# Kernel tuning notes

Measured on AMD Instinct MI355X. Metric: run time of the kernel, lower is better.

The kernel has to match this reference:

```python
import jax, jax.numpy as jnp
from jax import lax
import numpy as np

# GConv2d config (matches init_kwargs)
OUT_TRANSFORMS = 4  # rotations: 0, 90, 180, 270 degrees
STRIDE = 1
PADDING = 1


def setup_inputs() -> dict:
    key = jax.random.key(0)
    k1, k2, k3, k4 = jax.random.split(key, 4)
    B, IC_EFF, H, W = 16, 256, 64, 64   # IC_EFF = in_channels * in_transformations
    OC, K, F = 64, 4, 3                 # out_channels, num_dynamic_kernels, filter_size
    x = jax.random.normal(k1, (B, IC_EFF, H, W), dtype=jnp.float32)
    W_fc = jax.random.normal(k2, (K, IC_EFF), dtype=jnp.float32) * (1.0 / np.sqrt(IC_EFF))
    b_fc = jnp.zeros((K,), dtype=jnp.float32)
    kernel_bank = jax.random.normal(k3, (K, OC, IC_EFF, F, F), dtype=jnp.float32)
    return {"x": x, "W_fc": W_fc, "b_fc": b_fc, "kernel_bank": kernel_bank}


def reference(x, W_fc, b_fc, kernel_bank):
    B, C, H, W = x.shape
    # Dynamic routing: global average pool -> linear -> softmax over kernel bank
    pooled = x.mean(axis=(2, 3))                      # [B, C]
    coeffs = jax.nn.softmax(pooled @ W_fc.T + b_fc, axis=1)  # [B, K]
    # Sample-specific base kernels: mix of kernel bank
    base = jnp.einsum('bk,kocij->bocij', coeffs, kernel_bank)  # [B, oc, C, f, f]
    # P4 orientation expansion: rotate kernel spatially, stack along out-channels
    oriented = jnp.concatenate(
        [jnp.rot90(base, k, axes=(-2, -1)) for k in range(OUT_TRANSFORMS)], axis=1
    )  # [B, 4*oc, C, f, f]
    O, f = oriented.shape[1], oriented.shape[-1]
    # Batched per-sample conv via grouped convolution (one launch instead of B)
    xg = x.reshape(1, B * C, H, W)
    kg = oriented.reshape(B * O, C, f, f)
    out = lax.conv_general_dilated(
        xg, kg,
        window_strides=(STRIDE, STRIDE),
        padding=[(PADDING, PADDING), (PADDING, PADDING)],
        dimension_numbers=('NCHW', 'OIHW', 'NCHW'),
        feature_group_count=B,
    )  # [1, B*O, H', W']
    Ho, Wo = out.shape[-2], out.shape[-1]
    return out.reshape(B, O, Ho, Wo)
```

## Files before the change

kernel.cpp:

```cpp
#include <hip/hip_runtime.h>

#define B_  16
#define C_  256
#define OC_ 64
#define O_  256

typedef short    bf16x8 __attribute__((ext_vector_type(8)));
typedef float    f32x16 __attribute__((ext_vector_type(16)));
typedef unsigned u32x4  __attribute__((ext_vector_type(4)));
typedef unsigned u32x2  __attribute__((ext_vector_type(2)));

#define RT8   8
#define XR    10
#define XC    66
#define XTILE (XR*2*XC*8)
#define WTILE (9*2*64*8)
#define WORP_PER WTILE
#define WORP_BYTES ((size_t)B_*16*4*WORP_PER*2)

__device__ __forceinline__ unsigned cvtpk(float lo, float hi) {
    unsigned r;
    asm("v_cvt_pk_bf16_f32 %0, %1, %2" : "=v"(r) : "v"(lo), "v"(hi));
    return r;
}

__device__ __forceinline__ void gload16(const void* g, void* l) {
    __builtin_amdgcn_global_load_lds(
        (const __attribute__((address_space(1))) unsigned int*)g,
        (__attribute__((address_space(3))) unsigned int*)l, 16, 0, 0);
}

__global__ __launch_bounds__(256) void pool_kernel(const float* __restrict__ x,
                                                   float* __restrict__ pooled) {
    int bc = blockIdx.x;
    const float4* p = (const float4*)(x + (size_t)bc * 4096);
    float s = 0.f;
#pragma unroll
    for (int i = 0; i < 4; ++i) {
        float4 v = p[threadIdx.x + 256 * i];
        s += v.x + v.y + v.z + v.w;
    }
#pragma unroll
    for (int off = 32; off; off >>= 1) s += __shfl_down(s, off, 64);
    __shared__ float red[4];
    int lane = threadIdx.x & 63, wid = threadIdx.x >> 6;
    if (lane == 0) red[wid] = s;
    __syncthreads();
    if (threadIdx.x == 0)
        pooled[bc] = (red[0] + red[1] + red[2] + red[3]) * (1.0f / 4096.0f);
}

__global__ __launch_bounds__(256) void mix_kernel(const float* __restrict__ bank,
                                                  const float* __restrict__ pooled,
                                                  const float* __restrict__ W_fc,
                                                  const float* __restrict__ b_fc,
                                                  short* __restrict__ worp) {
    const int b  = blockIdx.x;
    const int cc = blockIdx.y;
    const int t  = threadIdx.x, lane = t & 63, wid = t >> 6;

    __shared__ float bankL[4 * 64 * 37];
    __shared__ float lg[4];

    {
        float s = 0.f;
#pragma unroll
        for (int q = 0; q < 4; ++q) {
            int c = lane * 4 + q;
            s += pooled[b * C_ + c] * W_fc[wid * C_ + c];
        }
#pragma unroll
        for (int off = 32; off; off >>= 1) s += __shfl_down(s, off, 64);
        if (lane == 0) lg[wid] = s + b_fc[wid];
    }
    __syncthreads();
    float l0 = lg[0], l1 = lg[1], l2 = lg[2], l3 = lg[3];
    float mx = fmaxf(fmaxf(l0, l1), fmaxf(l2, l3));
    float e0 = expf(l0 - mx), e1 = expf(l1 - mx), e2 = expf(l2 - mx), e3 = expf(l3 - mx);
    float inv = 1.f / (e0 + e1 + e2 + e3);
    const float cf0 = e0 * inv, cf1 = e1 * inv, cf2 = e2 * inv, cf3 = e3 * inv;

    const int oq  = t >> 6;
    const int o64 = t & 63;

    for (int sub = 0; sub < 4; ++sub) {
        __syncthreads();
        for (int i = t; i < 9216; i += 256) {
            int run = i / 36, e = i % 36;
            bankL[run * 37 + e] = bank[((size_t)run * C_ + cc * 16 + sub * 4) * 9 + e];
        }
        __syncthreads();

        const int lhs = sub >> 1;
        const float* bp = &bankL[o64 * 37];
#pragma unroll
        for (int ti = 0; ti < 3; ++ti)
#pragma unroll
            for (int tj = 0; tj < 3; ++tj) {
                int si, sj;
                if      (oq == 0) { si = ti;     sj = tj;     }
                else if (oq == 1) { si = tj;     sj = 2 - ti; }
                else if (oq == 2) { si = 2 - ti; sj = 2 - tj; }
                else              { si = 2 - tj; sj = ti;     }
                const int sij = si * 3 + sj;
                float v[4];
#pragma unroll
                for (int c4 = 0; c4 < 4; ++c4) {
                    const float* q = bp + c4 * 9 + sij;
                    v[c4] = cf0 * q[0] + cf1 * q[64 * 37] + cf2 * q[2 * 64 * 37]
                          + cf3 * q[3 * 64 * 37];
                }
                u32x2 d = { cvtpk(v[0], v[1]), cvtpk(v[2], v[3]) };
                size_t base = (((((size_t)(b * 16 + cc) * 4 + oq) * 9 + (ti * 3 + tj)) * 2
                                + lhs) * 64 + o64) * 8 + (sub & 1) * 4;
                *(u32x2*)&worp[base] = d;
            }
    }
}

__global__ __launch_bounds__(256, 2)
void conv_mfma(const float* __restrict__ x, const short* __restrict__ worp,
               float* __restrict__ out) {
    __shared__ short xls[XTILE];
    __shared__ short wls[2 * WTILE];

    const int g    = blockIdx.x;
    const int w    = (g & 7) * 64 + (g >> 3);
    const int oq   = w & 3;
    const int m    = w >> 2;
    const int rowt = m & 7;
    const int b    = m >> 3;
    const int y0   = rowt * RT8;

    const int t    = threadIdx.x;
    const int lane = t & 63;
    const int wid  = t >> 6;
    const int l31  = lane & 31;
    const int lh   = lane >> 5;

    const float* xb  = x + ((size_t)b << 20);
    const short* wbB = worp + ((size_t)(b * 16) * 4 + oq) * WORP_PER;

    int  goff[3], lb[3];
    bool act[3], inb[3];
#pragma unroll
    for (int si = 0; si < 3; ++si) {
        int s = t + si * 256;
        act[si] = (s < XR * XC);
        int r = s / XC, col = s % XC;
        int y = y0 + r - 1, gx = col - 1;
        inb[si]  = act[si] && (unsigned)y < 64 && (unsigned)gx < 64;
        goff[si] = y * 64 + gx;
        lb[si]   = ((r * 2) * XC + col) * 8;
    }
    float xf0[16], xf1[16], xf2[16];

#define LOADSLOT(xf, si, ccc)                                                   \
    { const float* p = xb + ((size_t)(ccc) << 16) + goff[si];                   \
      _Pragma("unroll")                                                         \
      for (int ci = 0; ci < 16; ++ci) xf[ci] = inb[si] ? p[(size_t)ci << 12] : 0.f; }

#define WRITESLOT(xf, si)                                                       \
    if (act[si]) {                                                              \
        u32x4 dA = { cvtpk(xf[0], xf[1]),  cvtpk(xf[2], xf[3]),                 \
                     cvtpk(xf[4], xf[5]),  cvtpk(xf[6], xf[7]) };               \
        u32x4 dB = { cvtpk(xf[8], xf[9]),  cvtpk(xf[10], xf[11]),               \
                     cvtpk(xf[12], xf[13]), cvtpk(xf[14], xf[15]) };            \
        *(u32x4*)&xls[lb[si]]          = dA;                                    \
        *(u32x4*)&xls[lb[si] + XC * 8] = dB;                                    \
    }

#define GLOADW(ccc, par)                                                        \
    { const char* wsrc = (const char*)(wbB + (size_t)(ccc) * (4 * WORP_PER));   \
      char* wdst = (char*)(wls + (par) * WTILE);                                \
      for (int u = wid; u < 18; u += 4)                                         \
          gload16(wsrc + u * 1024 + lane * 16, wdst + u * 1024); }

    f32x16 acc0[4] = {}, acc1[4] = {};

    GLOADW(0, 0);
    LOADSLOT(xf0, 0, 0); LOADSLOT(xf1, 1, 0); LOADSLOT(xf2, 2, 0);
    WRITESLOT(xf0, 0);   WRITESLOT(xf1, 1);   WRITESLOT(xf2, 2);
    __syncthreads();

    for (int cc = 0; cc < 16; ++cc) {
        const bool pre = (cc < 15);
        if (pre) {
            GLOADW(cc + 1, (cc + 1) & 1);
            LOADSLOT(xf0, 0, cc + 1);
            LOADSLOT(xf1, 1, cc + 1);
            LOADSLOT(xf2, 2, cc + 1);
        }
        const short* wcur = wls + (cc & 1) * WTILE;
#pragma unroll
        for (int i = 0; i < 3; ++i)
#pragma unroll
            for (int j = 0; j < 3; ++j) {
                const int tap = i * 3 + j;
                const short* wp = wcur + ((tap * 2 + lh) * 64 + l31) * 8;
                bf16x8 A0 = *(const bf16x8*)wp;
                bf16x8 A1 = *(const bf16x8*)(wp + 256);
#pragma unroll
                for (int pf = 0; pf < 4; ++pf) {
                    const int rr   = ((wid * 128 + pf * 32) >> 6) + i;
                    const int colb = ((wid * 128 + pf * 32) & 63) + j;
                    bf16x8 Bv = *(const bf16x8*)&xls[((rr * 2 + lh) * XC + colb + l31) * 8];
                    acc0[pf] = __builtin_amdgcn_mfma_f32_32x32x16_bf16(A0, Bv, acc0[pf], 0, 0, 0);
                    acc1[pf] = __builtin_amdgcn_mfma_f32_32x32x16_bf16(A1, Bv, acc1[pf], 0, 0, 0);
                }
            }
        __syncthreads();
        if (pre) {
            WRITESLOT(xf0, 0); WRITESLOT(xf1, 1); WRITESLOT(xf2, 2);
        }
        __syncthreads();
    }

#pragma unroll
    for (int pf = 0; pf < 4; ++pf) {
        const int yb  = y0 + 2 * wid + (pf >> 1);
        const int xcb = 32 * (pf & 1) + l31;
#pragma unroll
        for (int r = 0; r < 16; ++r) {
            const int orow = (r & 3) + 8 * (r >> 2) + 4 * lh;
            const int o0   = oq * 64 + orow;
            out[((size_t)(b * O_ + o0)      << 12) + yb * 64 + xcb] = acc0[pf][r];
            out[((size_t)(b * O_ + o0 + 32) << 12) + yb * 64 + xcb] = acc1[pf][r];
        }
    }
#undef LOADSLOT
#undef WRITESLOT
#undef GLOADW
}

extern "C" void kernel_launch(void* const* d_in, const int* in_sizes, int n_in,
                              void* d_out, int out_size, void* d_ws, size_t ws_size,
                              hipStream_t stream) {
    const float* x    = (const float*)d_in[0];
    const float* W_fc = (const float*)d_in[1];
    const float* b_fc = (const float*)d_in[2];
    const float* bank = (const float*)d_in[3];
    float* out = (float*)d_out;

    short* worp   = (short*)d_ws;
    float* pooled = (float*)((char*)d_ws + WORP_BYTES);

    pool_kernel<<<B_ * C_, 256, 0, stream>>>(x, pooled);
    mix_kernel<<<dim3(B_, 16), 256, 0, stream>>>(bank, pooled, W_fc, b_fc, worp);
    conv_mfma<<<512, 256, 0, stream>>>(x, worp, out);
}
```

Measured before the change: 123.5 us.

## Pre-transpose input to padded bf16 layout and stream conv tiles via direct LDS loads

The pooling kernel becomes an xprep kernel. It computes partial channel means and also writes x once as a zero-padded, channel-interleaved bf16 tensor in workspace. The conv kernel then double-buffers both the input and weight tiles with global_load_lds DMA instead of register loads, per-element conversion and LDS stores, which removes one barrier per iteration. It also raises wave priority around the MFMA loop. The cost is an extra global write and read of the transposed input and larger LDS usage.

```diff
diff --git a/kernel.cpp b/kernel.cpp
--- a/kernel.cpp
+++ b/kernel.cpp
@@ -2,7 +2,6 @@
 
 #define B_  16
 #define C_  256
-#define OC_ 64
 #define O_  256
 
 typedef short    bf16x8 __attribute__((ext_vector_type(8)));
@@ -10,13 +9,14 @@
 typedef unsigned u32x4  __attribute__((ext_vector_type(4)));
 typedef unsigned u32x2  __attribute__((ext_vector_type(2)));
 
-#define RT8   8
-#define XR    10
-#define XC    66
-#define XTILE (XR*2*XC*8)
-#define WTILE (9*2*64*8)
-#define WORP_PER WTILE
-#define WORP_BYTES ((size_t)B_*16*4*WORP_PER*2)
+#define XROW_SH  1056
+#define XBC_SH   (66 * XROW_SH)
+#define XT_BYTES ((size_t)B_ * 16 * XBC_SH * 2)
+
+#define WTILE_SH 9216
+#define WORP_BYTES ((size_t)B_ * 16 * 4 * WTILE_SH * 2)
+
+#define XBUF_SH  10752
 
 __device__ __forceinline__ unsigned cvtpk(float lo, float hi) {
     unsigned r;
@@ -30,28 +30,71 @@
         (__attribute__((address_space(3))) unsigned int*)l, 16, 0, 0);
 }
 
-__global__ __launch_bounds__(256) void pool_kernel(const float* __restrict__ x,
-                                                   float* __restrict__ pooled) {
-    int bc = blockIdx.x;
-    const float4* p = (const float4*)(x + (size_t)bc * 4096);
+__global__ __launch_bounds__(256) void xprep_kernel(const float* __restrict__ x,
+                                                    short* __restrict__ xT,
+                                                    float* __restrict__ pooled4) {
+    const int cc = blockIdx.x;
+    const int b  = blockIdx.y;
+    const int z  = blockIdx.z;
+    const int t  = threadIdx.x;
+
+    __shared__ float xsf[2][16][67];
+
+    short* xTb = xT + (size_t)(b * 16 + cc) * XBC_SH;
+    const float* xb = x + ((size_t)(b * C_ + cc * 16) << 12);
+
+    {
+        u32x4 zv = {0, 0, 0, 0};
+        int nz = 64 + ((z == 0 || z == 3) ? 132 : 0);
+        for (int i = t; i < nz; i += 256) {
+            int off;
+            if (i < 64) {
+                int row = z * 16 + 1 + (i >> 2);
+                int sub = i & 3;
+                off = row * XROW_SH + (sub >> 1) * 528 + ((sub & 1) ? 65 * 8 : 0);
+            } else {
+                off = (z == 0 ? 0 : 65 * XROW_SH) + (i - 64) * 8;
+            }
+            *(u32x4*)&xTb[off] = zv;
+        }
+    }
+
+    const int cl = t >> 4;
+    const int xq = t & 15;
     float s = 0.f;
-#pragma unroll
-    for (int i = 0; i < 4; ++i) {
-        float4 v = p[threadIdx.x + 256 * i];
-        s += v.x + v.y + v.z + v.w;
-    }
-#pragma unroll
-    for (int off = 32; off; off >>= 1) s += __shfl_down(s, off, 64);
-    __shared__ float red[4];
-    int lane = threadIdx.x & 63, wid = threadIdx.x >> 6;
-    if (lane == 0) red[wid] = s;
-    __syncthreads();
-    if (threadIdx.x == 0)
-        pooled[bc] = (red[0] + red[1] + red[2] + red[3]) * (1.0f / 4096.0f);
+
+    for (int it = 0; it < 8; ++it) {
+        const int ybase = z * 16 + it * 2;
+        const float* src = xb + ((size_t)cl << 12) + ybase * 64 + xq * 4;
+        float4 v0 = *(const float4*)src;
+        float4 v1 = *(const float4*)(src + 64);
+        s += v0.x + v0.y + v0.z + v0.w + v1.x + v1.y + v1.z + v1.w;
+        __syncthreads();
+        float* d0 = &xsf[0][cl][xq * 4];
+        d0[0] = v0.x; d0[1] = v0.y; d0[2] = v0.z; d0[3] = v0.w;
+        float* d1 = &xsf[1][cl][xq * 4];
+        d1[0] = v1.x; d1[1] = v1.y; d1[2] = v1.z; d1[3] = v1.w;
+        __syncthreads();
+        const int yy  = t >> 7;
+        const int lhh = (t >> 6) & 1;
+        const int col = (t & 63) + 1;
+        const float* rr = &xsf[yy][lhh * 8][col - 1];
+        u32x4 d;
+        d[0] = cvtpk(rr[0 * 67], rr[1 * 67]);
+        d[1] = cvtpk(rr[2 * 67], rr[3 * 67]);
+        d[2] = cvtpk(rr[4 * 67], rr[5 * 67]);
+        d[3] = cvtpk(rr[6 * 67], rr[7 * 67]);
+        *(u32x4*)&xTb[(ybase + yy + 1) * XROW_SH + lhh * 528 + col * 8] = d;
+    }
+
+#pragma unroll
+    for (int off = 1; off < 16; off <<= 1) s += __shfl_xor(s, off, 64);
+    if (xq == 0)
+        pooled4[(z * B_ + b) * C_ + cc * 16 + cl] = s * (1.0f / 4096.0f);
 }
 
 __global__ __launch_bounds__(256) void mix_kernel(const float* __restrict__ bank,
-                                                  const float* __restrict__ pooled,
+                                                  const float* __restrict__ pooled4,
                                                   const float* __restrict__ W_fc,
                                                   const float* __restrict__ b_fc,
                                                   short* __restrict__ worp) {
@@ -67,7 +110,9 @@
 #pragma unroll
         for (int q = 0; q < 4; ++q) {
             int c = lane * 4 + q;
-            s += pooled[b * C_ + c] * W_fc[wid * C_ + c];
+            float pv = pooled4[b * C_ + c] + pooled4[(B_ + b) * C_ + c]
+                     + pooled4[(2 * B_ + b) * C_ + c] + pooled4[(3 * B_ + b) * C_ + c];
+            s += pv * W_fc[wid * C_ + c];
         }
 #pragma unroll
         for (int off = 32; off; off >>= 1) s += __shfl_down(s, off, 64);
@@ -119,10 +164,9 @@
 }
 
 __global__ __launch_bounds__(256, 2)
-void conv_mfma(const float* __restrict__ x, const short* __restrict__ worp,
+void conv_mfma(const short* __restrict__ xT, const short* __restrict__ worp,
                float* __restrict__ out) {
-    __shared__ short xls[XTILE];
-    __shared__ short wls[2 * WTILE];
+    __shared__ short lds[2 * XBUF_SH + 2 * WTILE_SH];
 
     const int g    = blockIdx.x;
     const int w    = (g & 7) * 64 + (g >> 3);
@@ -130,7 +174,7 @@
     const int m    = w >> 2;
     const int rowt = m & 7;
     const int b    = m >> 3;
-    const int y0   = rowt * RT8;
+    const int y0   = rowt * 8;
 
     const int t    = threadIdx.x;
     const int lane = t & 63;
@@ -138,60 +182,30 @@
     const int l31  = lane & 31;
     const int lh   = lane >> 5;
 
-    const float* xb  = x + ((size_t)b << 20);
-    const short* wbB = worp + ((size_t)(b * 16) * 4 + oq) * WORP_PER;
-
-    int  goff[3], lb[3];
-    bool act[3], inb[3];
-#pragma unroll
-    for (int si = 0; si < 3; ++si) {
-        int s = t + si * 256;
-        act[si] = (s < XR * XC);
-        int r = s / XC, col = s % XC;
-        int y = y0 + r - 1, gx = col - 1;
-        inb[si]  = act[si] && (unsigned)y < 64 && (unsigned)gx < 64;
-        goff[si] = y * 64 + gx;
-        lb[si]   = ((r * 2) * XC + col) * 8;
-    }
-    float xf0[16], xf1[16], xf2[16];
-
-#define LOADSLOT(xf, si, ccc)                                                   \
-    { const float* p = xb + ((size_t)(ccc) << 16) + goff[si];                   \
-      _Pragma("unroll")                                                         \
-      for (int ci = 0; ci < 16; ++ci) xf[ci] = inb[si] ? p[(size_t)ci << 12] : 0.f; }
-
-#define WRITESLOT(xf, si)                                                       \
-    if (act[si]) {                                                              \
-        u32x4 dA = { cvtpk(xf[0], xf[1]),  cvtpk(xf[2], xf[3]),                 \
-                     cvtpk(xf[4], xf[5]),  cvtpk(xf[6], xf[7]) };               \
-        u32x4 dB = { cvtpk(xf[8], xf[9]),  cvtpk(xf[10], xf[11]),               \
-                     cvtpk(xf[12], xf[13]), cvtpk(xf[14], xf[15]) };            \
-        *(u32x4*)&xls[lb[si]]          = dA;                                    \
-        *(u32x4*)&xls[lb[si] + XC * 8] = dB;                                    \
-    }
-
-#define GLOADW(ccc, par)                                                        \
-    { const char* wsrc = (const char*)(wbB + (size_t)(ccc) * (4 * WORP_PER));   \
-      char* wdst = (char*)(wls + (par) * WTILE);                                \
-      for (int u = wid; u < 18; u += 4)                                         \
-          gload16(wsrc + u * 1024 + lane * 16, wdst + u * 1024); }
+    const char* xsrcB = (const char*)xT
+        + ((size_t)(b * 16) * XBC_SH + (size_t)y0 * XROW_SH) * 2 + lane * 16;
+    const char* wsrcB = (const char*)worp
+        + (((size_t)(b * 16) * 4) + oq) * (WTILE_SH * 2) + lane * 16;
+
+#define STAGE(ccc, p)                                                           \
+    { const char* xs = xsrcB + (size_t)(ccc) * (XBC_SH * 2);                    \
+      const char* ws = wsrcB + (size_t)(ccc) * (4 * WTILE_SH * 2);              \
+      char* xd = (char*)lds + (p) * (XBUF_SH * 2);                              \
+      char* wd = (char*)lds + 2 * (XBUF_SH * 2) + (p) * (WTILE_SH * 2);         \
+      for (int u = wid; u < 21; u += 4) gload16(xs + u * 1024, xd + u * 1024);  \
+      for (int u = wid; u < 18; u += 4) gload16(ws + u * 1024, wd + u * 1024); }
 
     f32x16 acc0[4] = {}, acc1[4] = {};
 
-    GLOADW(0, 0);
-    LOADSLOT(xf0, 0, 0); LOADSLOT(xf1, 1, 0); LOADSLOT(xf2, 2, 0);
-    WRITESLOT(xf0, 0);   WRITESLOT(xf1, 1);   WRITESLOT(xf2, 2);
+    STAGE(0, 0);
     __syncthreads();
 
     for (int cc = 0; cc < 16; ++cc) {
-        const bool pre = (cc < 15);
-        if (pre) {
-            GLOADW(cc + 1, (cc + 1) & 1);
-            LOADSLOT(xf0, 0, cc + 1);
-            LOADSLOT(xf1, 1, cc + 1);
-            LOADSLOT(xf2, 2, cc + 1);
-        }
-        const short* wcur = wls + (cc & 1) * WTILE;
+        const int p = cc & 1;
+        if (cc < 15) STAGE(cc + 1, p ^ 1);
+        const short* xcur = lds + p * XBUF_SH;
+        const short* wcur = lds + 2 * XBUF_SH + p * WTILE_SH;
+        __builtin_amdgcn_s_setprio(1);
 #pragma unroll
         for (int i = 0; i < 3; ++i)
 #pragma unroll
@@ -202,19 +216,18 @@
                 bf16x8 A1 = *(const bf16x8*)(wp + 256);
 #pragma unroll
                 for (int pf = 0; pf < 4; ++pf) {
-                    const int rr   = ((wid * 128 + pf * 32) >> 6) + i;
-                    const int colb = ((wid * 128 + pf * 32) & 63) + j;
-                    bf16x8 Bv = *(const bf16x8*)&xls[((rr * 2 + lh) * XC + colb + l31) * 8];
+                    const int rl   = 2 * wid + (pf >> 1) + i;
+                    const int colb = (pf & 1) * 32 + j;
+                    bf16x8 Bv = *(const bf16x8*)
+                        &xcur[((rl * 2 + lh) * 66 + colb + l31) * 8];
                     acc0[pf] = __builtin_amdgcn_mfma_f32_32x32x16_bf16(A0, Bv, acc0[pf], 0, 0, 0);
                     acc1[pf] = __builtin_amdgcn_mfma_f32_32x32x16_bf16(A1, Bv, acc1[pf], 0, 0, 0);
                 }
             }
-        __syncthreads();
-        if (pre) {
-            WRITESLOT(xf0, 0); WRITESLOT(xf1, 1); WRITESLOT(xf2, 2);
-        }
-        __syncthreads();
-    }
+        __builtin_amdgcn_s_setprio(0);
+        __syncthreads();
+    }
+#undef STAGE
 
 #pragma unroll
     for (int pf = 0; pf < 4; ++pf) {
@@ -228,9 +241,6 @@
             out[((size_t)(b * O_ + o0 + 32) << 12) + yb * 64 + xcb] = acc1[pf][r];
         }
     }
-#undef LOADSLOT
-#undef WRITESLOT
-#undef GLOADW
 }
 
 extern "C" void kernel_launch(void* const* d_in, const int* in_sizes, int n_in,
@@ -242,10 +252,11 @@
     const float* bank = (const float*)d_in[3];
     float* out = (float*)d_out;
 
-    short* worp   = (short*)d_ws;
-    float* pooled = (float*)((char*)d_ws + WORP_BYTES);
-
-    pool_kernel<<<B_ * C_, 256, 0, stream>>>(x, pooled);
-    mix_kernel<<<dim3(B_, 16), 256, 0, stream>>>(bank, pooled, W_fc, b_fc, worp);
-    conv_mfma<<<512, 256, 0, stream>>>(x, worp, out);
-}
+    short* xTb     = (short*)d_ws;
+    short* worp    = (short*)((char*)d_ws + XT_BYTES);
+    float* pooled4 = (float*)((char*)d_ws + XT_BYTES + WORP_BYTES);
+
+    xprep_kernel<<<dim3(16, 16, 4), 256, 0, stream>>>(x, xTb, pooled4);
+    mix_kernel<<<dim3(B_, 16), 256, 0, stream>>>(bank, pooled4, W_fc, b_fc, worp);
+    conv_mfma<<<512, 256, 0, stream>>>(xTb, worp, out);
+}
```

Measured after the change: 112.7 us. 1.1x faster.
